# Kernel tuning notes

Hardware: AMD Instinct MI355X
Metric: run time of the kernel (lower is better)

The kernel has to match this reference:

```python
import jax, jax.numpy as jnp
import numpy as np

NF = 64        # num_feat
DG = 16        # deformable_groups
K = 3
KK = K * K
CG = NF // DG  # channels per deformable group


def lrelu(x):
    return jnp.where(x >= 0, x, 0.1 * x)


def conv3x3(x, w, b):
    y = jax.lax.conv_general_dilated(
        x, w, window_strides=(1, 1), padding=((1, 1), (1, 1)),
        dimension_numbers=('NCHW', 'OIHW', 'NCHW'))
    return y + b[None, :, None, None]


def _bilinear(feat, py, px):
    # feat: (C, H, W); py, px: arbitrary shape S -> (C,) + S; zeros outside bounds
    H, W = feat.shape[-2:]
    y0f = jnp.floor(py)
    x0f = jnp.floor(px)
    dy = py - y0f
    dx = px - x0f
    y0 = y0f.astype(jnp.int32)
    x0 = x0f.astype(jnp.int32)
    out = jnp.zeros(feat.shape[:1] + py.shape, feat.dtype)
    for yy, xx, wgt in ((y0, x0, (1 - dy) * (1 - dx)),
                        (y0, x0 + 1, (1 - dy) * dx),
                        (y0 + 1, x0, dy * (1 - dx)),
                        (y0 + 1, x0 + 1, dy * dx)):
        valid = (yy >= 0) & (yy < H) & (xx >= 0) & (xx < W)
        v = feat[:, jnp.clip(yy, 0, H - 1), jnp.clip(xx, 0, W - 1)]
        out = out + v * (wgt * valid)[None]
    return out


def backwarp(x, flow):
    # x: (N,C,H,W); flow: (N,2,H,W) with channels (dx, dy) in pixels
    N, C, H, W = x.shape
    gy, gx = jnp.meshgrid(jnp.arange(H, dtype=x.dtype),
                          jnp.arange(W, dtype=x.dtype), indexing='ij')
    px = gx[None] + flow[:, 0]
    py = gy[None] + flow[:, 1]
    return jax.vmap(_bilinear)(x, py, px)


def dcn_v2(x, offset, mask, w, b):
    # x: (N,C,H,W); offset: (N, DG*KK*2, H, W) as consecutive (dy,dx) pairs;
    # mask: (N, DG*KK, H, W) already sigmoided. stride=1, pad=1, k=3.
    N, C, H, W = x.shape
    off = offset.reshape(N, DG, KK, 2, H, W)
    dy, dx = off[:, :, :, 0], off[:, :, :, 1]            # (N,DG,KK,H,W)
    gy, gx = jnp.meshgrid(jnp.arange(H, dtype=x.dtype),
                          jnp.arange(W, dtype=x.dtype), indexing='ij')
    ky = (jnp.arange(KK) // K - K // 2).astype(x.dtype)  # tap row offset: -1,0,1
    kx = (jnp.arange(KK) % K - K // 2).astype(x.dtype)   # tap col offset
    py = dy + gy[None, None, None] + ky[None, None, :, None, None]
    px = dx + gx[None, None, None] + kx[None, None, :, None, None]
    xg = x.reshape(N, DG, CG, H, W)
    sampled = jax.vmap(jax.vmap(_bilinear))(xg, py, px)  # (N,DG,CG,KK,H,W)
    sampled = sampled * mask.reshape(N, DG, 1, KK, H, W)
    wr = w.reshape(-1, DG, CG, KK)                       # (Cout,DG,CG,KK)
    out = jnp.einsum('ngckhw,ogck->nohw', sampled, wr)
    return out + b[None, :, None, None]


def fgda(nbr_feat, ref_feat, flow, w1, b1, w2, b2, w3, b3, w4, b4, dcn_w, dcn_b):
    warped = backwarp(nbr_feat, flow)
    h = lrelu(conv3x3(jnp.concatenate([warped, ref_feat], axis=1), w1, b1))
    h = lrelu(conv3x3(h, w2, b2))
    h = lrelu(conv3x3(h, w3, b3))
    out = conv3x3(h, w4, b4)                             # (N, DG*27, H, W)
    o1, o2, mask = jnp.split(out, 3, axis=1)
    N, _, H, W = flow.shape
    residual = jnp.concatenate([o1, o2], axis=1).reshape(N, -1, 2, H, W)
    # torch.flip(flow, dims=[1]) -> (flow_y, flow_x), broadcast over all taps
    offset = flow[:, ::-1].reshape(N, 1, 2, H, W) + residual
    offset = offset.reshape(N, -1, H, W)
    mask = jax.nn.sigmoid(mask)
    return lrelu(dcn_v2(nbr_feat, offset, mask, dcn_w, dcn_b))


def setup_inputs():
    key = jax.random.key(0)
    ks = jax.random.split(key, 8)
    N, H, W = 8, 128, 128
    s = 0.05
    return {
        'nbr_feat': jax.random.normal(ks[0], (N, NF, H, W), jnp.float32),
        'ref_feat': jax.random.normal(ks[1], (N, NF, H, W), jnp.float32),
        'flow': jax.random.normal(ks[2], (N, 2, H, W), jnp.float32) * 2.0,
        'w1': jax.random.normal(ks[3], (NF, 2 * NF, 3, 3), jnp.float32) * s,
        'b1': jnp.zeros((NF,), jnp.float32),
        'w2': jax.random.normal(ks[4], (NF, NF, 3, 3), jnp.float32) * s,
        'b2': jnp.zeros((NF,), jnp.float32),
        'w3': jax.random.normal(ks[5], (NF, NF, 3, 3), jnp.float32) * s,
        'b3': jnp.zeros((NF,), jnp.float32),
        'w4': jax.random.normal(ks[6], (DG * 3 * KK, NF, 3, 3), jnp.float32) * s,
        'b4': jnp.zeros((DG * 3 * KK,), jnp.float32),
        'dcn_w': jax.random.normal(ks[7], (NF, NF, 3, 3), jnp.float32) * s,
        'dcn_b': jnp.zeros((NF,), jnp.float32),
    }


def reference(nbr_feat, ref_feat, flow, w1, b1, w2, b2, w3, b3, w4, b4, dcn_w, dcn_b):
    return fgda(nbr_feat, ref_feat, flow, w1, b1, w2, b2, w3, b3, w4, b4, dcn_w, dcn_b)
```

## Files before the change

kernel.cpp:

```cpp
#include <hip/hip_runtime.h>
#include <math.h>

#define H 128
#define W 128
#define NB 8
#define NFC 64

typedef __attribute__((ext_vector_type(8))) short s16x8;
typedef __attribute__((ext_vector_type(4))) short s16x4;
typedef __attribute__((ext_vector_type(4))) float f32x4;
typedef __attribute__((ext_vector_type(4))) int   i32x4;
typedef __attribute__((ext_vector_type(2))) int   i32x2;

__device__ __forceinline__ float b2f(short s) {
    return __uint_as_float(((unsigned)(unsigned short)s) << 16);
}
__device__ __forceinline__ short f2bf(float f) {
    unsigned u = __float_as_uint(f);
    u += 0x7FFF + ((u >> 16) & 1);
    return (short)(u >> 16);
}
__device__ __forceinline__ short f2h(float f) {
    _Float16 h = (_Float16)f;
    return __builtin_bit_cast(short, h);
}
__device__ __forceinline__ float h2f(short s) {
    return (float)__builtin_bit_cast(_Float16, s);
}

__global__ __launch_bounds__(256) void k_wt_all(
    const float* __restrict__ w1, const float* __restrict__ w2,
    const float* __restrict__ w3, const float* __restrict__ w4,
    const float* __restrict__ dcw, short* __restrict__ wp)
{
    int idx = blockIdx.x * 256 + threadIdx.x;
    int u = idx / 576;
    int r = idx - u * 576;
    int t = r >> 6, i = r & 63;
    float v;
    if (u < 128) {
        int o = u & 63, icoff = (u >> 6) << 6;
        v = w1[((size_t)(o * 128) + icoff + i) * 9 + t];
    } else if (u < 192) {
        int o = u - 128;
        v = w2[((size_t)(o * 64) + i) * 9 + t];
    } else if (u < 256) {
        int o = u - 192;
        v = w3[((size_t)(o * 64) + i) * 9 + t];
    } else if (u < 704) {
        int o = u - 256;
        v = (o < 432) ? w4[((size_t)(o * 64) + i) * 9 + t] : 0.f;
    } else {
        int o = u - 704;
        v = dcw[((size_t)(o * 64) + i) * 9 + t];
    }
    wp[idx] = f2bf(v);
}

__global__ __launch_bounds__(256) void k_nhwc2(const float* __restrict__ nbr,
                                               const float* __restrict__ ref,
                                               short* __restrict__ nbrG,
                                               short* __restrict__ refH)
{
    int px = blockIdx.x * 256 + threadIdx.x;
    bool isNbr = (px < 131072);
    const float* src;
    if (isNbr) { src = nbr; }
    else       { src = ref; px -= 131072; }
    int n = px >> 14;
    int sp = px & 16383;
    const float* s = src + (size_t)n * 64 * 16384 + sp;
    unsigned pk[32];
    #pragma unroll
    for (int c = 0; c < 32; ++c) {
        float v0 = s[(size_t)(2 * c) * 16384];
        float v1 = s[(size_t)(2 * c + 1) * 16384];
        pk[c] = (unsigned)(unsigned short)f2bf(v0) |
                ((unsigned)(unsigned short)f2bf(v1) << 16);
    }
    if (isNbr) {
        #pragma unroll
        for (int g = 0; g < 16; ++g) {
            i32x2 t;
            t[0] = pk[2 * g]; t[1] = pk[2 * g + 1];
            *(i32x2*)(nbrG + ((size_t)(n * 16 + g) * 16384 + sp) * 4) = t;
        }
    } else {
        i32x4* d = (i32x4*)(refH + (size_t)(n * 16384 + sp) * 64);
        #pragma unroll
        for (int qq = 0; qq < 8; ++qq) {
            i32x4 t;
            t[0] = pk[4 * qq]; t[1] = pk[4 * qq + 1];
            t[2] = pk[4 * qq + 2]; t[3] = pk[4 * qq + 3];
            d[qq] = t;
        }
    }
}

__global__ __launch_bounds__(256) void k_backwarp(const short* __restrict__ nbrG,
                                                  const float* __restrict__ flow,
                                                  short* __restrict__ warped)
{
    int idx = blockIdx.x * 256 + threadIdx.x;
    int px = idx >> 2, qt = idx & 3;
    int n = px >> 14;
    int x = px & 127, y = (px >> 7) & 127;
    float fx = flow[(size_t)(n * 2 + 0) * 16384 + y * 128 + x];
    float fy = flow[(size_t)(n * 2 + 1) * 16384 + y * 128 + x];
    float pxf = (float)x + fx, pyf = (float)y + fy;
    float x0f = floorf(pxf), y0f = floorf(pyf);
    int x0 = (int)x0f, y0 = (int)y0f;
    float dx = pxf - x0f, dy = pyf - y0f;
    float vy0 = ((unsigned)y0 < 128u) ? 1.f : 0.f;
    float vy1 = ((unsigned)(y0 + 1) < 128u) ? 1.f : 0.f;
    float vx0 = ((unsigned)x0 < 128u) ? 1.f : 0.f;
    float vx1 = ((unsigned)(x0 + 1) < 128u) ? 1.f : 0.f;
    float w00 = (1.f - dy) * (1.f - dx) * vy0 * vx0;
    float w01 = (1.f - dy) * dx * vy0 * vx1;
    float w10 = dy * (1.f - dx) * vy1 * vx0;
    float w11 = dy * dx * vy1 * vx1;
    int y0c = min(max(y0, 0), 127), y1c = min(max(y0 + 1, 0), 127);
    int x0c = min(max(x0, 0), 127), x1c = min(max(x0 + 1, 0), 127);
    int xb = min(max(x0, 0), 126);
    bool s0 = (x0c == xb), s1 = (x1c == xb);

    const short* plbase = nbrG + (size_t)n * 16 * 65536;
    s16x8 r0, r1;
    #pragma unroll
    for (int pg = 0; pg < 4; ++pg) {
        const short* pl = plbase + (size_t)(qt * 4 + pg) * 65536;
        s16x8 p0 = *(const s16x8*)(pl + (y0c * 128 + xb) * 4);
        s16x8 p1 = *(const s16x8*)(pl + (y1c * 128 + xb) * 4);
        #pragma unroll
        for (int cc = 0; cc < 4; ++cc) {
            float v00 = b2f(s0 ? p0[cc] : p0[4 + cc]);
            float v01 = b2f(s1 ? p0[cc] : p0[4 + cc]);
            float v10 = b2f(s0 ? p1[cc] : p1[4 + cc]);
            float v11 = b2f(s1 ? p1[cc] : p1[4 + cc]);
            float v = w00 * v00 + w01 * v01 + w10 * v10 + w11 * v11;
            short res = f2bf(v);
            if (pg < 2) r0[pg * 4 + cc] = res;
            else        r1[(pg - 2) * 4 + cc] = res;
        }
    }
    short* o = warped + (size_t)px * 64 + qt * 16;
    *(s16x8*)o = r0;
    *(s16x8*)(o + 8) = r1;
}

template<int MODE>
__global__ __launch_bounds__(256) void k_conv(
    const short* __restrict__ in, const short* __restrict__ wT,
    const float* __restrict__ bias,
    float* __restrict__ partial, short* __restrict__ outB,
    int* __restrict__ offP, short* __restrict__ maskP,
    const float* __restrict__ flow, int n0)
{
    __shared__ __align__(16) short tileS[324 * 64];
    __shared__ __align__(16) short aS[64 * 64];

    int tid = threadIdx.x;
    int bid = blockIdx.x;
    int og = (MODE == 3) ? blockIdx.y : 0;
    int n  = (MODE == 3) ? (n0 + (bid >> 6)) : (bid >> 6);
    int tl = bid & 63;
    int bx = (tl & 7) << 4;
    int by = (tl >> 3) << 4;
    int ln = tid & 63, wv = tid >> 6;
    int c = ln & 15, q = ln >> 4;

    for (int i = tid; i < 2592; i += 256) {
        int pt = i >> 3, c16 = i & 7;
        int ty = pt / 18, tx = pt - ty * 18;
        int gy = by + ty - 1, gx = bx + tx - 1;
        i32x4 v = {0, 0, 0, 0};
        if ((unsigned)gy < 128u && (unsigned)gx < 128u)
            v = *(const i32x4*)(in + (((size_t)n * 128 + gy) * 128 + gx) * 64 + c16 * 8);
        *(i32x4*)((char*)tileS + pt * 128 + ((c16 ^ (pt & 7)) << 4)) = v;
    }

    const short* wbase = wT + ((MODE == 3) ? (size_t)og * 36864 : 0);
    int aoc = tid >> 3, ac8 = tid & 7;
    i32x4 sa0 = *(const i32x4*)(wbase + (size_t)aoc * 576 + ac8 * 8);
    i32x4 sa1 = *(const i32x4*)(wbase + (size_t)(aoc + 32) * 576 + ac8 * 8);

    f32x4 acc[4][4];
    #pragma unroll
    for (int m = 0; m < 4; ++m)
        #pragma unroll
        for (int p = 0; p < 4; ++p)
            acc[m][p] = (f32x4){0.f, 0.f, 0.f, 0.f};

    int cy = c >> 2, cx = c & 3;

    __syncthreads();

    for (int tap = 0; tap < 9; ++tap) {
        *(i32x4*)((char*)aS + aoc * 128 + ((ac8 ^ (aoc & 7)) << 4)) = sa0;
        *(i32x4*)((char*)aS + (aoc + 32) * 128 + ((ac8 ^ ((aoc + 32) & 7)) << 4)) = sa1;
        if (tap < 8) {
            sa0 = *(const i32x4*)(wbase + (size_t)aoc * 576 + (tap + 1) * 64 + ac8 * 8);
            sa1 = *(const i32x4*)(wbase + (size_t)(aoc + 32) * 576 + (tap + 1) * 64 + ac8 * 8);
        }
        __syncthreads();

        int dty = tap / 3, dtx = tap - dty * 3;
        int ptr0 = (wv * 4 + cy + dty) * 18 + cx + dtx;
        #pragma unroll
        for (int ih = 0; ih < 2; ++ih) {
            int slot = ih * 4 + q;
            s16x8 bf[4];
            #pragma unroll
            for (int p = 0; p < 4; ++p) {
                int ptp = ptr0 + p * 4;
                bf[p] = *(const s16x8*)((const char*)tileS + ptp * 128 + ((slot ^ (ptp & 7)) << 4));
            }
            #pragma unroll
            for (int m = 0; m < 4; ++m) {
                int ocl = m * 16 + c;
                s16x8 a = *(const s16x8*)((const char*)aS + ocl * 128 + ((slot ^ (ocl & 7)) << 4));
                #pragma unroll
                for (int p = 0; p < 4; ++p)
                    acc[m][p] = __builtin_amdgcn_mfma_f32_16x16x32_bf16(a, bf[p], acc[m][p], 0, 0, 0);
            }
        }
        __syncthreads();
    }

    #pragma unroll
    for (int p = 0; p < 4; ++p) {
        int y = by + wv * 4 + cy;
        int x = bx + p * 4 + cx;
        size_t pxi = ((size_t)n * 128 + y) * 128 + x;
        float fy = 0.f, fx2 = 0.f;
        if (MODE == 3) {
            fy  = flow[(size_t)(n * 2 + 1) * 16384 + y * 128 + x];
            fx2 = flow[(size_t)(n * 2 + 0) * 16384 + y * 128 + x];
        }
        #pragma unroll
        for (int m = 0; m < 4; ++m) {
            int o0 = m * 16 + q * 4;
            f32x4 v = acc[m][p];
            if (MODE == 0) {
                *(f32x4*)(partial + pxi * 64 + o0) = v;
            } else if (MODE == 1 || MODE == 2) {
                f32x4 bv = *(const f32x4*)(bias + o0);
                if (MODE == 1) {
                    f32x4 pv = *(const f32x4*)(partial + pxi * 64 + o0);
                    v += pv;
                }
                v += bv;
                s16x4 r;
                #pragma unroll
                for (int j = 0; j < 4; ++j) {
                    float t = v[j];
                    t = t >= 0.f ? t : 0.1f * t;
                    r[j] = f2bf(t);
                }
                *(s16x4*)(outB + pxi * 64 + o0) = r;
            } else {
                int oc4 = og * 64 + o0;
                if (oc4 < 432) {
                    f32x4 bv = *(const f32x4*)(bias + oc4);
                    v += bv;
                    size_t nrel = (size_t)(bid >> 6);
                    int pxl = y * 128 + x;
                    if (oc4 < 288) {
                        int gk0 = oc4 >> 1;
                        int g0 = gk0 / 9, t0 = gk0 - g0 * 9;
                        int gk1 = gk0 + 1;
                        int g1 = gk1 / 9, t1 = gk1 - g1 * 9;
                        unsigned pk0 = (unsigned)(unsigned short)f2h(v[0] + fy) |
                                       ((unsigned)(unsigned short)f2h(v[1] + fx2) << 16);
                        unsigned pk1 = (unsigned)(unsigned short)f2h(v[2] + fy) |
                                       ((unsigned)(unsigned short)f2h(v[3] + fx2) << 16);
                        offP[(((nrel * 9 + t0) * 4 + (g0 >> 2)) * 16384 + (size_t)pxl) * 4 + (g0 & 3)] = (int)pk0;
                        offP[(((nrel * 9 + t1) * 4 + (g1 >> 2)) * 16384 + (size_t)pxl) * 4 + (g1 & 3)] = (int)pk1;
                    } else {
                        int gkb = oc4 - 288;
                        #pragma unroll
                        for (int j = 0; j < 4; ++j) {
                            int gk = gkb + j;
                            int g = gk / 9, t = gk - g * 9;
                            maskP[(((nrel * 9 + t) * 4 + (g >> 2)) * 16384 + (size_t)pxl) * 4 + (g & 3)] =
                                f2h(1.f / (1.f + expf(-v[j])));
                        }
                    }
                }
            }
        }
    }
}

__global__ __launch_bounds__(256) void k_dcn(
    const int* __restrict__ offP, const short* __restrict__ maskP,
    const short* __restrict__ nbrG, const short* __restrict__ dcwT,
    const float* __restrict__ dcb, float* __restrict__ out, int n0)
{
    __shared__ __align__(16) short smp[64 * 64];
    __shared__ __align__(16) short aS[64 * 64];

    int tid = threadIdx.x;
    int bid = blockIdx.x;
    int nrel = bid >> 8;
    int rb = bid & 255;
    int y = rb >> 1;
    int xh = (rb & 1) << 6;
    int n = n0 + nrel;

    int xt = tid & 63;
    int sg = tid >> 6;
    int ln = tid & 63, c = ln & 15, q = ln >> 4;
    int x = xh + xt;
    int pxl = y * 128 + x;

    int aoc = tid >> 3, ac8 = tid & 7;
    i32x4 sa0 = *(const i32x4*)(dcwT + (size_t)aoc * 576 + ac8 * 8);
    i32x4 sa1 = *(const i32x4*)(dcwT + (size_t)(aoc + 32) * 576 + ac8 * 8);

    const short* plg0 = nbrG + (size_t)(n * 16 + sg * 4) * 65536;

    f32x4 acc[4];
    #pragma unroll
    for (int m = 0; m < 4; ++m) acc[m] = (f32x4){0.f, 0.f, 0.f, 0.f};

    int brow = sg * 16 + c;

    for (int tap = 0; tap < 9; ++tap) {
        int dty = tap / 3 - 1, dtx = tap - (tap / 3) * 3 - 1;
        size_t obase = (((size_t)(nrel * 9 + tap) * 4 + sg) * 16384 + pxl) * 4;
        i32x4 dd4 = *(const i32x4*)(offP + obase);
        s16x4 mk4 = *(const s16x4*)(maskP + obase);

        s16x8 r01[2];
        #pragma unroll
        for (int gg = 0; gg < 4; ++gg) {
            float dyv = h2f((short)(dd4[gg] & 0xffff));
            float dxv = h2f((short)(((unsigned)dd4[gg]) >> 16));
            float mk  = h2f(mk4[gg]);
            float sy = (float)(y + dty) + dyv;
            float sx = (float)(x + dtx) + dxv;
            float y0f = floorf(sy), x0f = floorf(sx);
            int y0 = (int)y0f, x0 = (int)x0f;
            float ddy = sy - y0f, ddx = sx - x0f;
            float vy0 = ((unsigned)y0 < 128u) ? 1.f : 0.f;
            float vy1 = ((unsigned)(y0 + 1) < 128u) ? 1.f : 0.f;
            float vx0 = ((unsigned)x0 < 128u) ? 1.f : 0.f;
            float vx1 = ((unsigned)(x0 + 1) < 128u) ? 1.f : 0.f;
            float w00 = (1.f - ddy) * (1.f - ddx) * vy0 * vx0;
            float w01 = (1.f - ddy) * ddx * vy0 * vx1;
            float w10 = ddy * (1.f - ddx) * vy1 * vx0;
            float w11 = ddy * ddx * vy1 * vx1;
            int y0c = min(max(y0, 0), 127), y1c = min(max(y0 + 1, 0), 127);
            int x0c = min(max(x0, 0), 127), x1c = min(max(x0 + 1, 0), 127);
            int xb = min(max(x0, 0), 126);
            bool sel0 = (x0c == xb), sel1 = (x1c == xb);
            const short* plg = plg0 + (size_t)gg * 65536;
            s16x8 pr0 = *(const s16x8*)(plg + (y0c * 128 + xb) * 4);
            s16x8 pr1 = *(const s16x8*)(plg + (y1c * 128 + xb) * 4);
            #pragma unroll
            for (int cc = 0; cc < 4; ++cc) {
                float v00 = b2f(sel0 ? pr0[cc] : pr0[4 + cc]);
                float v01 = b2f(sel1 ? pr0[cc] : pr0[4 + cc]);
                float v10 = b2f(sel0 ? pr1[cc] : pr1[4 + cc]);
                float v11 = b2f(sel1 ? pr1[cc] : pr1[4 + cc]);
                float sv = w00 * v00 + w01 * v01 + w10 * v10 + w11 * v11;
                r01[gg >> 1][(gg & 1) * 4 + cc] = f2bf(sv * mk);
            }
        }
        *(s16x8*)((char*)smp + xt * 128 + (((sg * 2 + 0) ^ (xt & 7)) << 4)) = r01[0];
        *(s16x8*)((char*)smp + xt * 128 + (((sg * 2 + 1) ^ (xt & 7)) << 4)) = r01[1];
        *(i32x4*)((char*)aS + aoc * 128 + ((ac8 ^ (aoc & 7)) << 4)) = sa0;
        *(i32x4*)((char*)aS + (aoc + 32) * 128 + ((ac8 ^ ((aoc + 32) & 7)) << 4)) = sa1;
        if (tap < 8) {
            sa0 = *(const i32x4*)(dcwT + (size_t)aoc * 576 + (tap + 1) * 64 + ac8 * 8);
            sa1 = *(const i32x4*)(dcwT + (size_t)(aoc + 32) * 576 + (tap + 1) * 64 + ac8 * 8);
        }
        __syncthreads();

        #pragma unroll
        for (int ih = 0; ih < 2; ++ih) {
            int slot = ih * 4 + q;
            s16x8 bf = *(const s16x8*)((const char*)smp + brow * 128 + ((slot ^ (brow & 7)) << 4));
            #pragma unroll
            for (int m = 0; m < 4; ++m) {
                int ocl = m * 16 + c;
                s16x8 a = *(const s16x8*)((const char*)aS + ocl * 128 + ((slot ^ (ocl & 7)) << 4));
                acc[m] = __builtin_amdgcn_mfma_f32_16x16x32_bf16(a, bf, acc[m], 0, 0, 0);
            }
        }
        __syncthreads();
    }

    #pragma unroll
    for (int m = 0; m < 4; ++m) {
        int o0 = m * 16 + q * 4;
        f32x4 bv = *(const f32x4*)(dcb + o0);
        f32x4 v = acc[m] + bv;
        int xo = xh + sg * 16 + c;
        #pragma unroll
        for (int j = 0; j < 4; ++j) {
            float t = v[j];
            t = t >= 0.f ? t : 0.1f * t;
            out[((size_t)n * 64 + o0 + j) * 16384 + y * 128 + xo] = t;
        }
    }
}

extern "C" void kernel_launch(void* const* d_in, const int* in_sizes, int n_in,
                              void* d_out, int out_size, void* d_ws, size_t ws_size,
                              hipStream_t stream)
{
    const float* nbr  = (const float*)d_in[0];
    const float* ref  = (const float*)d_in[1];
    const float* flow = (const float*)d_in[2];
    const float* w1   = (const float*)d_in[3];
    const float* b1   = (const float*)d_in[4];
    const float* w2   = (const float*)d_in[5];
    const float* b2   = (const float*)d_in[6];
    const float* w3   = (const float*)d_in[7];
    const float* b3   = (const float*)d_in[8];
    const float* w4   = (const float*)d_in[9];
    const float* b4   = (const float*)d_in[10];
    const float* dcw  = (const float*)d_in[11];
    const float* dcb  = (const float*)d_in[12];
    float* out = (float*)d_out;
    char* ws = (char*)d_ws;

    short* nbrG   = (short*)ws;
    short* wpool  = (short*)(ws + 16777216);
    short* warped = (short*)(ws + 17825792);
    short* refH   = (short*)(ws + 34603008);
    float* h1p    = (float*)(ws + 51380224);
    int*   offP   = (int*)(ws + 17825792);
    short* maskP  = (short*)(ws + 55574528);
    short* h3     = (short*)(ws + 74448896);
    short* h1     = warped;
    short* h2     = refH;

    short* wT1a = wpool;
    short* wT1b = wpool + 36864;
    short* wT2  = wpool + 73728;
    short* wT3  = wpool + 110592;
    short* wT4  = wpool + 147456;
    short* dcwT = wpool + 405504;

    k_wt_all<<<1728, 256, 0, stream>>>(w1, w2, w3, w4, dcw, wpool);
    k_nhwc2<<<1024, 256, 0, stream>>>(nbr, ref, nbrG, refH);
    k_backwarp<<<2048, 256, 0, stream>>>(nbrG, flow, warped);

    k_conv<0><<<512, 256, 0, stream>>>(warped, wT1a, nullptr, h1p, nullptr, nullptr, nullptr, nullptr, 0);
    k_conv<1><<<512, 256, 0, stream>>>(refH, wT1b, b1, h1p, h1, nullptr, nullptr, nullptr, 0);
    k_conv<2><<<512, 256, 0, stream>>>(h1, wT2, b2, nullptr, h2, nullptr, nullptr, nullptr, 0);
    k_conv<2><<<512, 256, 0, stream>>>(h2, wT3, b3, nullptr, h3, nullptr, nullptr, nullptr, 0);

    for (int n0 = 0; n0 < 8; n0 += 4) {
        dim3 g4(256, 7);
        k_conv<3><<<g4, 256, 0, stream>>>(h3, wT4, b4, nullptr, nullptr, offP, maskP, flow, n0);
        k_dcn<<<1024, 256, 0, stream>>>(offP, maskP, nbrG, dcwT, dcb, out, n0);
    }
}
```

Measured before the change: 361.1 us.

## Prepack conv weights in MFMA fragment order and load A operands directly to registers

The weight-pack kernel now writes conv weights in the exact per-lane MFMA A-fragment order (tap, k-half, m-block, lane, 8 elements). The conv kernel then loads each lane's A fragments straight from global memory into registers, double-buffered across taps. This removes the shared-memory weight staging buffer and the two block-wide barriers per tap. In exchange each wave redundantly fetches the full weight slice from global/L2 and register pressure rises from the 16 extra vector registers.

```diff
diff --git a/kernel.cpp b/kernel.cpp
--- a/kernel.cpp
+++ b/kernel.cpp
@@ -34,24 +34,31 @@
     const float* __restrict__ dcw, short* __restrict__ wp)
 {
     int idx = blockIdx.x * 256 + threadIdx.x;
-    int u = idx / 576;
-    int r = idx - u * 576;
-    int t = r >> 6, i = r & 63;
     float v;
-    if (u < 128) {
-        int o = u & 63, icoff = (u >> 6) << 6;
-        v = w1[((size_t)(o * 128) + icoff + i) * 9 + t];
-    } else if (u < 192) {
-        int o = u - 128;
-        v = w2[((size_t)(o * 64) + i) * 9 + t];
-    } else if (u < 256) {
-        int o = u - 192;
-        v = w3[((size_t)(o * 64) + i) * 9 + t];
-    } else if (u < 704) {
-        int o = u - 256;
-        v = (o < 432) ? w4[((size_t)(o * 64) + i) * 9 + t] : 0.f;
+    if (idx < 405504) {
+        int ob = idx / 36864;
+        int rr = idx - ob * 36864;
+        int tap = rr >> 12;
+        int r3 = rr & 4095;
+        int ih = r3 >> 11;
+        int m = (r3 >> 9) & 3;
+        int ln = (r3 >> 3) & 63;
+        int e = r3 & 7;
+        int ocl = m * 16 + (ln & 15);
+        int ic = ih * 32 + (ln >> 4) * 8 + e;
+        if (ob == 0)      v = w1[((size_t)(ocl * 128) + ic) * 9 + tap];
+        else if (ob == 1) v = w1[((size_t)(ocl * 128) + 64 + ic) * 9 + tap];
+        else if (ob == 2) v = w2[((size_t)(ocl * 64) + ic) * 9 + tap];
+        else if (ob == 3) v = w3[((size_t)(ocl * 64) + ic) * 9 + tap];
+        else {
+            int oc4 = (ob - 4) * 64 + ocl;
+            v = (oc4 < 432) ? w4[((size_t)(oc4 * 64) + ic) * 9 + tap] : 0.f;
+        }
     } else {
-        int o = u - 704;
+        int r = idx - 405504;
+        int o = r / 576;
+        int r2 = r - o * 576;
+        int t = r2 >> 6, i = r2 & 63;
         v = dcw[((size_t)(o * 64) + i) * 9 + t];
     }
     wp[idx] = f2bf(v);
@@ -157,7 +164,6 @@
     const float* __restrict__ flow, int n0)
 {
     __shared__ __align__(16) short tileS[324 * 64];
-    __shared__ __align__(16) short aS[64 * 64];
 
     int tid = threadIdx.x;
     int bid = blockIdx.x;
@@ -180,9 +186,13 @@
     }
 
     const short* wbase = wT + ((MODE == 3) ? (size_t)og * 36864 : 0);
-    int aoc = tid >> 3, ac8 = tid & 7;
-    i32x4 sa0 = *(const i32x4*)(wbase + (size_t)aoc * 576 + ac8 * 8);
-    i32x4 sa1 = *(const i32x4*)(wbase + (size_t)(aoc + 32) * 576 + ac8 * 8);
+
+    s16x8 A[8];
+    #pragma unroll
+    for (int f = 0; f < 8; ++f) {
+        int ih = f >> 2, m = f & 3;
+        A[f] = *(const s16x8*)(wbase + (((0 + ih) * 4 + m) * 64 + ln) * 8);
+    }
 
     f32x4 acc[4][4];
     #pragma unroll
@@ -195,36 +205,35 @@
 
     __syncthreads();
 
+    #pragma unroll
     for (int tap = 0; tap < 9; ++tap) {
-        *(i32x4*)((char*)aS + aoc * 128 + ((ac8 ^ (aoc & 7)) << 4)) = sa0;
-        *(i32x4*)((char*)aS + (aoc + 32) * 128 + ((ac8 ^ ((aoc + 32) & 7)) << 4)) = sa1;
+        s16x8 An[8];
         if (tap < 8) {
-            sa0 = *(const i32x4*)(wbase + (size_t)aoc * 576 + (tap + 1) * 64 + ac8 * 8);
-            sa1 = *(const i32x4*)(wbase + (size_t)(aoc + 32) * 576 + (tap + 1) * 64 + ac8 * 8);
-        }
-        __syncthreads();
-
+            #pragma unroll
+            for (int f = 0; f < 8; ++f) {
+                int ih = f >> 2, m = f & 3;
+                An[f] = *(const s16x8*)(wbase + ((((tap + 1) * 2 + ih) * 4 + m) * 64 + ln) * 8);
+            }
+        }
         int dty = tap / 3, dtx = tap - dty * 3;
         int ptr0 = (wv * 4 + cy + dty) * 18 + cx + dtx;
         #pragma unroll
         for (int ih = 0; ih < 2; ++ih) {
-            int slot = ih * 4 + q;
             s16x8 bf[4];
             #pragma unroll
             for (int p = 0; p < 4; ++p) {
                 int ptp = ptr0 + p * 4;
+                int slot = ih * 4 + q;
                 bf[p] = *(const s16x8*)((const char*)tileS + ptp * 128 + ((slot ^ (ptp & 7)) << 4));
             }
             #pragma unroll
-            for (int m = 0; m < 4; ++m) {
-                int ocl = m * 16 + c;
-                s16x8 a = *(const s16x8*)((const char*)aS + ocl * 128 + ((slot ^ (ocl & 7)) << 4));
+            for (int m = 0; m < 4; ++m)
                 #pragma unroll
                 for (int p = 0; p < 4; ++p)
-                    acc[m][p] = __builtin_amdgcn_mfma_f32_16x16x32_bf16(a, bf[p], acc[m][p], 0, 0, 0);
-            }
-        }
-        __syncthreads();
+                    acc[m][p] = __builtin_amdgcn_mfma_f32_16x16x32_bf16(A[ih * 4 + m], bf[p], acc[m][p], 0, 0, 0);
+        }
+        #pragma unroll
+        for (int f = 0; f < 8; ++f) A[f] = An[f];
     }
 
     #pragma unroll
```

New measurement: 439.8 us. 1.22x slower.
